# Optimization experiments

Hardware: AMD Instinct MI355X
Metric: run time of the kernel (lower is better)

The kernel has to match this reference:

```python
import jax, jax.numpy as jnp
import numpy as np

HIDDEN = 512
N_LAYERS = 2
SEQ = 512
BATCH = 64
H2 = HIDDEN * 2  # 1024
D_IN = H2 * (N_LAYERS + 1)  # 3072


def setup_inputs() -> dict:
    key = jax.random.key(0)
    ks = jax.random.split(key, 4)
    state = jax.random.normal(ks[0], (N_LAYERS, BATCH, H2), dtype=jnp.float32)
    encoder_output = jax.random.normal(ks[1], (SEQ, BATCH, H2), dtype=jnp.float32)
    # fc1: xavier_normal with tanh gain (5/3); fc2: kaiming_normal
    xavier_std = (5.0 / 3.0) * np.sqrt(2.0 / (D_IN + H2))
    W1 = jax.random.normal(ks[2], (H2, D_IN), dtype=jnp.float32) * xavier_std
    b1 = jnp.zeros((H2,), dtype=jnp.float32)
    W2 = jax.random.normal(ks[3], (1, H2), dtype=jnp.float32) * np.sqrt(2.0 / H2)
    b2 = jnp.zeros((1,), dtype=jnp.float32)
    return {"state": state, "encoder_output": encoder_output,
            "W1": W1, "b1": b1, "W2": W2, "b2": b2}


def reference(state, encoder_output, W1, b1, W2, b2):
    S, B, h2 = encoder_output.shape
    # (n_layers, B, H2) -> (B, n_layers*H2), broadcast over seq
    st = jnp.transpose(state, (1, 0, 2)).reshape(B, -1)
    st = jnp.broadcast_to(st[:, None, :], (B, S, st.shape[-1]))
    enc = jnp.transpose(encoder_output, (1, 0, 2))  # (B, S, H2)
    concat = jnp.concatenate([st, enc], axis=2)      # (B, S, 3*H2)
    energy = jnp.tanh(jnp.einsum('bsd,hd->bsh', concat, W1) + b1)
    energy = (jnp.einsum('bsh,oh->bso', energy, W2) + b2)  # (B, S, 1)
    energy = jnp.transpose(energy, (0, 2, 1))        # (B, 1, S)
    alpha = jax.nn.softmax(energy, axis=2)           # (B, 1, S)
    context = jnp.einsum('bqs,bsh->qbh', alpha, enc)  # (1, B, H2)
    return context, alpha
```

## Files before the change

### kernel.cpp

```cpp
#include <hip/hip_runtime.h>
#include <hip/hip_bf16.h>
#include <stdint.h>

#define H2      1024
#define SEQ     512
#define BATCH   64
#define M_TOTAL (SEQ * BATCH)

typedef __attribute__((ext_vector_type(8))) short short8;
typedef __attribute__((ext_vector_type(4))) float f32x4;

__device__ __forceinline__ unsigned pack2_bf16(float lo, float hi) {
    union { __hip_bfloat162 h; unsigned u; } v;
    v.h = __float22bfloat162_rn(make_float2(lo, hi));
    return v.u;
}

__device__ __forceinline__ float fast_tanh(float x) {
    float e = __expf(2.0f * x);
    return __fdividef(e - 1.0f, e + 1.0f);
}

__device__ __forceinline__ void gl_lds16(const unsigned short* g, unsigned short* l) {
    __builtin_amdgcn_global_load_lds(
        (const __attribute__((address_space(1))) unsigned int*)g,
        (__attribute__((address_space(3))) unsigned int*)l, 16, 0, 0);
}


__global__ __launch_bounds__(256) void k_setup(const float* __restrict__ W1,
                                               const float* __restrict__ b1,
                                               const float* __restrict__ state,
                                               const float* __restrict__ enc,
                                               unsigned short* __restrict__ W1e,
                                               unsigned short* __restrict__ encb,
                                               float* __restrict__ logits,
                                               float* __restrict__ sp,
                                               int swz) {
    int blk = blockIdx.x, tid = threadIdx.x;
    int lane = tid & 63;
    if (blk < 512) {
        if (swz) {
            int gr = blk * 4 + (tid >> 6);
            int L  = ((lane & 3) << 4) | (lane >> 2);
            int h  = ((gr >> 5) << 4) + (L & 15);
            int k  = ((gr & 31) << 5) + ((L >> 4) << 3);
            const float* src = W1 + (size_t)h * 3072 + 2048 + k;
            float4 v0 = *(const float4*)(src);
            float4 v1 = *(const float4*)(src + 4);
            uint4 o;
            o.x = pack2_bf16(v0.x, v0.y); o.y = pack2_bf16(v0.z, v0.w);
            o.z = pack2_bf16(v1.x, v1.y); o.w = pack2_bf16(v1.z, v1.w);
            *(uint4*)(W1e + (size_t)gr * 512 + L * 8) = o;
        } else {
            int i = blk * 256 + tid;
            int e = i << 3;
            int h = e >> 10, k = e & 1023;
            const float* src = W1 + (size_t)h * 3072 + 2048 + k;
            float4 v0 = *(const float4*)(src);
            float4 v1 = *(const float4*)(src + 4);
            uint4 o;
            o.x = pack2_bf16(v0.x, v0.y); o.y = pack2_bf16(v0.z, v0.w);
            o.z = pack2_bf16(v1.x, v1.y); o.w = pack2_bf16(v1.z, v1.w);
            *(uint4*)(W1e + ((size_t)h << 10) + k) = o;
        }
    } else if (blk < 640) {
        logits[(blk - 512) * 256 + tid] = 0.f;
    } else if (blk < 704) {
        int mT   = blk - 640;
        int wave = tid >> 6;
        int c    = lane & 15;
        int kq   = (lane >> 4) << 3;
        int h    = mT * 16 + c;
        int b    = wave * 16 + c;
        const float* ap = W1 + (size_t)h * 3072 + kq;
        f32x4 acc = {0.f, 0.f, 0.f, 0.f};
        #pragma unroll 4
        for (int k0 = 0; k0 < 2048; k0 += 32) {
            int k = k0 + kq;
            float4 a0 = *(const float4*)(ap + k0);
            float4 a1 = *(const float4*)(ap + k0 + 4);
            int l = k >> 10, j = k & 1023;
            const float* bp = state + (((size_t)l * 64 + b) << 10) + j;
            float4 b0 = *(const float4*)bp;
            float4 b1v = *(const float4*)(bp + 4);
            union { short8 s; uint4 u; } fa, fb;
            fa.u.x = pack2_bf16(a0.x, a0.y); fa.u.y = pack2_bf16(a0.z, a0.w);
            fa.u.z = pack2_bf16(a1.x, a1.y); fa.u.w = pack2_bf16(a1.z, a1.w);
            fb.u.x = pack2_bf16(b0.x, b0.y); fb.u.y = pack2_bf16(b0.z, b0.w);
            fb.u.z = pack2_bf16(b1v.x, b1v.y); fb.u.w = pack2_bf16(b1v.z, b1v.w);
            acc = __builtin_amdgcn_mfma_f32_16x16x32_bf16(fa.s, fb.s, acc, 0, 0, 0);
        }
        int quad = lane >> 4;
        int bcol = wave * 16 + c;
        #pragma unroll
        for (int i = 0; i < 4; ++i) {
            int hh = mT * 16 + quad * 4 + i;
            sp[((size_t)bcol << 10) + hh] = acc[i] + b1[hh];
        }
    } else {
        int gr = (blk - 704) * 4 + (tid >> 6);
        int L  = ((lane & 3) << 4) | (lane >> 2);
        int m  = ((gr >> 5) << 4) + (L & 15);
        int k  = ((gr & 31) << 5) + ((L >> 4) << 3);
        const float* src = enc + (size_t)m * 1024 + k;
        float4 v0 = *(const float4*)(src);
        float4 v1 = *(const float4*)(src + 4);
        uint4 o;
        o.x = pack2_bf16(v0.x, v0.y); o.y = pack2_bf16(v0.z, v0.w);
        o.z = pack2_bf16(v1.x, v1.y); o.w = pack2_bf16(v1.z, v1.w);
        *(uint4*)(encb + (size_t)gr * 512 + L * 8) = o;
    }
}

#define BM 128
#define BN 128
#define BK 32

__global__ __launch_bounds__(256, 2) void k_energy(const unsigned short* __restrict__ encb,
                                                   const unsigned short* __restrict__ W1e,
                                                   const float* __restrict__ sp,
                                                   const float* __restrict__ W2,
                                                   float* __restrict__ logits) {
    __shared__ unsigned short As[BM * BK];
    __shared__ unsigned short Bs[BN * BK];
    int bid = blockIdx.x;
    int c8  = bid & 7;
    int jj  = bid >> 3;
    int mT  = c8 * 32 + (jj >> 3);
    int nT  = jj & 7;
    int n0  = nT * BN;
    int m0  = mT * BM;
    int tid  = threadIdx.x;
    int lane = tid & 63, wave = tid >> 6;
    int wm   = (wave >> 1) << 6;
    int wn   = (wave & 1) << 6;

    int rg0 = wave * 2, rg1 = wave * 2 + 1;
    const unsigned short* gA0 = encb + ((size_t)(mT * 8 + rg0) * 32) * 512 + lane * 8;
    const unsigned short* gA1 = encb + ((size_t)(mT * 8 + rg1) * 32) * 512 + lane * 8;
    const unsigned short* gB0 = W1e  + ((size_t)(nT * 8 + rg0) * 32) * 512 + lane * 8;
    const unsigned short* gB1 = W1e  + ((size_t)(nT * 8 + rg1) * 32) * 512 + lane * 8;
    unsigned short* lA0 = As + rg0 * 512;
    unsigned short* lA1 = As + rg1 * 512;
    unsigned short* lB0 = Bs + rg0 * 512;
    unsigned short* lB1 = Bs + rg1 * 512;

    f32x4 acc[4][4];
    #pragma unroll
    for (int mi = 0; mi < 4; ++mi)
        #pragma unroll
        for (int ni = 0; ni < 4; ++ni)
            acc[mi][ni] = (f32x4){0.f, 0.f, 0.f, 0.f};

    int ablk = wm >> 4;
    int bblk = wn >> 4;
    const unsigned short* afb = As + ablk * 512 + lane * 8;
    const unsigned short* bfb = Bs + bblk * 512 + lane * 8;

    for (int k0 = 0; k0 < H2; k0 += BK) {
        int go = k0 * 16;
        __syncthreads();
        gl_lds16(gA0 + go, lA0);
        gl_lds16(gA1 + go, lA1);
        gl_lds16(gB0 + go, lB0);
        gl_lds16(gB1 + go, lB1);
        __syncthreads();
        short8 af[4], bf[4];
        #pragma unroll
        for (int i = 0; i < 4; ++i) {
            af[i] = *(const short8*)(afb + i * 512);
            bf[i] = *(const short8*)(bfb + i * 512);
        }
        #pragma unroll
        for (int mi = 0; mi < 4; ++mi)
            #pragma unroll
            for (int ni = 0; ni < 4; ++ni)
                acc[mi][ni] = __builtin_amdgcn_mfma_f32_16x16x32_bf16(af[mi], bf[ni], acc[mi][ni], 0, 0, 0);
    }

    int c    = lane & 15;
    int quad = lane >> 4;
    float w2v[4];
    int   hcol[4];
    #pragma unroll
    for (int ni = 0; ni < 4; ++ni) {
        hcol[ni] = n0 + wn + ni * 16 + c;
        w2v[ni]  = W2[hcol[ni]];
    }
    #pragma unroll
    for (int mi = 0; mi < 4; ++mi) {
        #pragma unroll
        for (int i = 0; i < 4; ++i) {
            int m = m0 + wm + mi * 16 + quad * 4 + i;
            int b = m & 63;
            const float* sprow = sp + ((size_t)b << 10);
            float t = 0.f;
            #pragma unroll
            for (int ni = 0; ni < 4; ++ni) {
                float e = acc[mi][ni][i] + sprow[hcol[ni]];
                t = fmaf(fast_tanh(e), w2v[ni], t);
            }
            t += __shfl_xor(t, 1);
            t += __shfl_xor(t, 2);
            t += __shfl_xor(t, 4);
            t += __shfl_xor(t, 8);
            if (c == 0) atomicAdd(logits + (size_t)b * 512 + (m >> 6), t);
        }
    }
}

#define LDT 40
__global__ __launch_bounds__(256, 2) void k_energy_f32(const float* __restrict__ enc,
                                                       const unsigned short* __restrict__ W1e,
                                                       const float* __restrict__ sp,
                                                       const float* __restrict__ W2,
                                                       float* __restrict__ logits) {
    __shared__ unsigned short As[BM * LDT];
    __shared__ unsigned short Bs[BN * LDT];
    int bid = blockIdx.x;
    int c8  = bid & 7;
    int jj  = bid >> 3;
    int mT  = c8 * 32 + (jj >> 3);
    int nT  = jj & 7;
    int tid  = threadIdx.x;
    int lane = tid & 63, wave = tid >> 6;
    int wm   = (wave >> 1) << 6;
    int wn   = (wave & 1) << 6;
    int m0   = mT * BM, n0 = nT * BN;

    int arow = tid >> 1;
    int aseg = (tid & 1) << 4;
    const float*          apg = enc + ((size_t)(m0 + arow) << 10) + aseg;
    const unsigned short* wpg = W1e + ((size_t)(n0 + arow) << 10) + aseg;
    unsigned short* asd = As + arow * LDT + aseg;
    unsigned short* bsd = Bs + arow * LDT + aseg;

    f32x4 acc[4][4];
    #pragma unroll
    for (int mi = 0; mi < 4; ++mi)
        #pragma unroll
        for (int ni = 0; ni < 4; ++ni)
            acc[mi][ni] = (f32x4){0.f, 0.f, 0.f, 0.f};

    int c  = lane & 15;
    int kq = (lane >> 4) << 3;
    const unsigned short* afp = As + (wm + c) * LDT + kq;
    const unsigned short* bfp = Bs + (wn + c) * LDT + kq;

    for (int k0 = 0; k0 < 1024; k0 += 32) {
        float4 a0 = *(const float4*)(apg + k0);
        float4 a1 = *(const float4*)(apg + k0 + 4);
        float4 a2 = *(const float4*)(apg + k0 + 8);
        float4 a3 = *(const float4*)(apg + k0 + 12);
        uint4  w0 = *(const uint4*)(wpg + k0);
        uint4  w1 = *(const uint4*)(wpg + k0 + 8);
        uint4 pa0, pa1;
        pa0.x = pack2_bf16(a0.x, a0.y); pa0.y = pack2_bf16(a0.z, a0.w);
        pa0.z = pack2_bf16(a1.x, a1.y); pa0.w = pack2_bf16(a1.z, a1.w);
        pa1.x = pack2_bf16(a2.x, a2.y); pa1.y = pack2_bf16(a2.z, a2.w);
        pa1.z = pack2_bf16(a3.x, a3.y); pa1.w = pack2_bf16(a3.z, a3.w);
        __syncthreads();
        *(uint4*)asd       = pa0;
        *(uint4*)(asd + 8) = pa1;
        *(uint4*)bsd       = w0;
        *(uint4*)(bsd + 8) = w1;
        __syncthreads();
        short8 af[4], bf[4];
        #pragma unroll
        for (int i = 0; i < 4; ++i) {
            af[i] = *(const short8*)(afp + (i << 4) * LDT);
            bf[i] = *(const short8*)(bfp + (i << 4) * LDT);
        }
        #pragma unroll
        for (int mi = 0; mi < 4; ++mi)
            #pragma unroll
            for (int ni = 0; ni < 4; ++ni)
                acc[mi][ni] = __builtin_amdgcn_mfma_f32_16x16x32_bf16(af[mi], bf[ni], acc[mi][ni], 0, 0, 0);
    }

    int quad = lane >> 4;
    float w2v[4];
    int   hcol[4];
    #pragma unroll
    for (int ni = 0; ni < 4; ++ni) {
        hcol[ni] = n0 + wn + ni * 16 + c;
        w2v[ni]  = W2[hcol[ni]];
    }
    #pragma unroll
    for (int mi = 0; mi < 4; ++mi) {
        #pragma unroll
        for (int i = 0; i < 4; ++i) {
            int m = m0 + wm + mi * 16 + quad * 4 + i;
            int b = m & 63;
            const float* sprow = sp + ((size_t)b << 10);
            float t = 0.f;
            #pragma unroll
            for (int ni = 0; ni < 4; ++ni) {
                float e = acc[mi][ni][i] + sprow[hcol[ni]];
                t = fmaf(fast_tanh(e), w2v[ni], t);
            }
            t += __shfl_xor(t, 1);
            t += __shfl_xor(t, 2);
            t += __shfl_xor(t, 4);
            t += __shfl_xor(t, 8);
            if (c == 0) atomicAdd(logits + (size_t)b * 512 + (m >> 6), t);
        }
    }
}

__global__ __launch_bounds__(256) void k_softmax(const float* __restrict__ logits,
                                                 float* __restrict__ alpha,
                                                 float* __restrict__ ctx) {
    int b = blockIdx.x;
    int tid = threadIdx.x;
    int lane = tid & 63, wave = tid >> 6;
    #pragma unroll
    for (int j = 0; j < 4; ++j)
        ctx[((size_t)b << 10) + j * 256 + tid] = 0.f;
    float v0 = logits[(size_t)b * 512 + tid];
    float v1 = logits[(size_t)b * 512 + 256 + tid];
    float mx = fmaxf(v0, v1);
    #pragma unroll
    for (int o = 32; o; o >>= 1) mx = fmaxf(mx, __shfl_xor(mx, o));
    __shared__ float redm[4];
    if (lane == 0) redm[wave] = mx;
    __syncthreads();
    mx = fmaxf(fmaxf(redm[0], redm[1]), fmaxf(redm[2], redm[3]));
    float e0 = __expf(v0 - mx), e1 = __expf(v1 - mx);
    float s = e0 + e1;
    #pragma unroll
    for (int o = 32; o; o >>= 1) s += __shfl_xor(s, o);
    __shared__ float reds[4];
    if (lane == 0) reds[wave] = s;
    __syncthreads();
    s = reds[0] + reds[1] + reds[2] + reds[3];
    float inv = 1.0f / s;
    alpha[(size_t)b * 512 + tid]       = e0 * inv;
    alpha[(size_t)b * 512 + 256 + tid] = e1 * inv;
}

__global__ __launch_bounds__(256) void k_context(const float* __restrict__ enc,
                                                 const float* __restrict__ alpha,
                                                 float* __restrict__ ctx) {
    int b  = blockIdx.x & 63;
    int sc = blockIdx.x >> 6;
    int h  = threadIdx.x << 2;
    float4 acc = make_float4(0.f, 0.f, 0.f, 0.f);
    int sbase = sc * 64;
    #pragma unroll 4
    for (int si = 0; si < 64; ++si) {
        int s = sbase + si;
        float a = alpha[(size_t)b * 512 + s];
        float4 e = *(const float4*)(enc + (((size_t)s * 64 + b) << 10) + h);
        acc.x = fmaf(a, e.x, acc.x);
        acc.y = fmaf(a, e.y, acc.y);
        acc.z = fmaf(a, e.z, acc.z);
        acc.w = fmaf(a, e.w, acc.w);
    }
    float* dst = ctx + ((size_t)b << 10) + h;
    atomicAdd(dst + 0, acc.x);
    atomicAdd(dst + 1, acc.y);
    atomicAdd(dst + 2, acc.z);
    atomicAdd(dst + 3, acc.w);
}

extern "C" void kernel_launch(void* const* d_in, const int* in_sizes, int n_in,
                              void* d_out, int out_size, void* d_ws, size_t ws_size,
                              hipStream_t stream) {
    const float* state = (const float*)d_in[0];
    const float* enc   = (const float*)d_in[1];
    const float* W1    = (const float*)d_in[2];
    const float* b1    = (const float*)d_in[3];
    const float* W2    = (const float*)d_in[4];

    float* ctx   = (float*)d_out;
    float* alpha = (float*)d_out + 65536;

    char* ws = (char*)d_ws;
    unsigned short* W1e    = (unsigned short*)(ws);
    float*          sp     = (float*)(ws + 2097152);
    float*          logits = (float*)(ws + 2097152 + 262144);
    unsigned short* encb   = (unsigned short*)(ws + 2097152 + 262144 + 131072);

    const size_t need_full = 2097152 + 262144 + 131072 + (size_t)M_TOTAL * H2 * 2;
    bool full = ws_size >= need_full;

    k_setup<<<full ? 17088 : 704, 256, 0, stream>>>(W1, b1, state, enc, W1e, encb,
                                                    logits, sp, full ? 1 : 0);
    if (full) {
        k_energy<<<M_TOTAL / BM * (H2 / BN), 256, 0, stream>>>(encb, W1e, sp, W2, logits);
    } else {
        k_energy_f32<<<M_TOTAL / BM * (H2 / BN), 256, 0, stream>>>(enc, W1e, sp, W2, logits);
    }
    k_softmax<<<64, 256, 0, stream>>>(logits, alpha, ctx);
    k_context<<<512, 256, 0, stream>>>(enc, alpha, ctx);
}
```

Baseline: 384.3 us.

## Fuse fp32-to-bf16 conversion of encoder output into energy GEMM A-tile loads

Removes the separate pass in the setup kernel that converted the full encoder output (64 MB fp32) into a swizzled bf16 buffer. The energy GEMM now reads fp32 encoder rows directly, converts them to bf16 in registers and writes them to LDS, with next-iteration A loads issued as register prefetch to overlap the MFMA work. This drops a 64 MB read plus 32 MB write round trip, but each energy block now reads fp32 A (twice the bytes, repeated across the 8 N-tiles) and adds conversion ALU work inside the main loop. The fallback fp32 energy kernel and the workspace-size switch are removed.

New measurement: 436.4 us. 13.5% more time.

```diff
diff --git a/kernel.cpp b/kernel.cpp
--- a/kernel.cpp
+++ b/kernel.cpp
@@ -31,42 +31,26 @@
 __global__ __launch_bounds__(256) void k_setup(const float* __restrict__ W1,
                                                const float* __restrict__ b1,
                                                const float* __restrict__ state,
-                                               const float* __restrict__ enc,
                                                unsigned short* __restrict__ W1e,
-                                               unsigned short* __restrict__ encb,
                                                float* __restrict__ logits,
-                                               float* __restrict__ sp,
-                                               int swz) {
+                                               float* __restrict__ sp) {
     int blk = blockIdx.x, tid = threadIdx.x;
     int lane = tid & 63;
     if (blk < 512) {
-        if (swz) {
-            int gr = blk * 4 + (tid >> 6);
-            int L  = ((lane & 3) << 4) | (lane >> 2);
-            int h  = ((gr >> 5) << 4) + (L & 15);
-            int k  = ((gr & 31) << 5) + ((L >> 4) << 3);
-            const float* src = W1 + (size_t)h * 3072 + 2048 + k;
-            float4 v0 = *(const float4*)(src);
-            float4 v1 = *(const float4*)(src + 4);
-            uint4 o;
-            o.x = pack2_bf16(v0.x, v0.y); o.y = pack2_bf16(v0.z, v0.w);
-            o.z = pack2_bf16(v1.x, v1.y); o.w = pack2_bf16(v1.z, v1.w);
-            *(uint4*)(W1e + (size_t)gr * 512 + L * 8) = o;
-        } else {
-            int i = blk * 256 + tid;
-            int e = i << 3;
-            int h = e >> 10, k = e & 1023;
-            const float* src = W1 + (size_t)h * 3072 + 2048 + k;
-            float4 v0 = *(const float4*)(src);
-            float4 v1 = *(const float4*)(src + 4);
-            uint4 o;
-            o.x = pack2_bf16(v0.x, v0.y); o.y = pack2_bf16(v0.z, v0.w);
-            o.z = pack2_bf16(v1.x, v1.y); o.w = pack2_bf16(v1.z, v1.w);
-            *(uint4*)(W1e + ((size_t)h << 10) + k) = o;
-        }
+        int gr = blk * 4 + (tid >> 6);
+        int L  = ((lane & 3) << 4) | (lane >> 2);
+        int h  = ((gr >> 5) << 4) + (L & 15);
+        int k  = ((gr & 31) << 5) + ((L >> 4) << 3);
+        const float* src = W1 + (size_t)h * 3072 + 2048 + k;
+        float4 v0 = *(const float4*)(src);
+        float4 v1 = *(const float4*)(src + 4);
+        uint4 o;
+        o.x = pack2_bf16(v0.x, v0.y); o.y = pack2_bf16(v0.z, v0.w);
+        o.z = pack2_bf16(v1.x, v1.y); o.w = pack2_bf16(v1.z, v1.w);
+        *(uint4*)(W1e + (size_t)gr * 512 + L * 8) = o;
     } else if (blk < 640) {
         logits[(blk - 512) * 256 + tid] = 0.f;
-    } else if (blk < 704) {
+    } else {
         int mT   = blk - 640;
         int wave = tid >> 6;
         int c    = lane & 15;
@@ -98,18 +82,6 @@
             int hh = mT * 16 + quad * 4 + i;
             sp[((size_t)bcol << 10) + hh] = acc[i] + b1[hh];
         }
-    } else {
-        int gr = (blk - 704) * 4 + (tid >> 6);
-        int L  = ((lane & 3) << 4) | (lane >> 2);
-        int m  = ((gr >> 5) << 4) + (L & 15);
-        int k  = ((gr & 31) << 5) + ((L >> 4) << 3);
-        const float* src = enc + (size_t)m * 1024 + k;
-        float4 v0 = *(const float4*)(src);
-        float4 v1 = *(const float4*)(src + 4);
-        uint4 o;
-        o.x = pack2_bf16(v0.x, v0.y); o.y = pack2_bf16(v0.z, v0.w);
-        o.z = pack2_bf16(v1.x, v1.y); o.w = pack2_bf16(v1.z, v1.w);
-        *(uint4*)(encb + (size_t)gr * 512 + L * 8) = o;
     }
 }
 
@@ -117,7 +89,7 @@
 #define BN 128
 #define BK 32
 
-__global__ __launch_bounds__(256, 2) void k_energy(const unsigned short* __restrict__ encb,
+__global__ __launch_bounds__(256, 2) void k_energy(const float* __restrict__ enc,
                                                    const unsigned short* __restrict__ W1e,
                                                    const float* __restrict__ sp,
                                                    const float* __restrict__ W2,
@@ -137,12 +109,15 @@
     int wn   = (wave & 1) << 6;
 
     int rg0 = wave * 2, rg1 = wave * 2 + 1;
-    const unsigned short* gA0 = encb + ((size_t)(mT * 8 + rg0) * 32) * 512 + lane * 8;
-    const unsigned short* gA1 = encb + ((size_t)(mT * 8 + rg1) * 32) * 512 + lane * 8;
-    const unsigned short* gB0 = W1e  + ((size_t)(nT * 8 + rg0) * 32) * 512 + lane * 8;
-    const unsigned short* gB1 = W1e  + ((size_t)(nT * 8 + rg1) * 32) * 512 + lane * 8;
-    unsigned short* lA0 = As + rg0 * 512;
-    unsigned short* lA1 = As + rg1 * 512;
+    int arow0 = m0 + rg0 * 16 + (lane & 15);
+    int arow1 = m0 + rg1 * 16 + (lane & 15);
+    int akoff = (lane >> 4) << 3;
+    const float* gA0 = enc + (size_t)arow0 * 1024 + akoff;
+    const float* gA1 = enc + (size_t)arow1 * 1024 + akoff;
+    const unsigned short* gB0 = W1e + ((size_t)(nT * 8 + rg0) * 32) * 512 + lane * 8;
+    const unsigned short* gB1 = W1e + ((size_t)(nT * 8 + rg1) * 32) * 512 + lane * 8;
+    unsigned short* lA0 = As + rg0 * 512 + lane * 8;
+    unsigned short* lA1 = As + rg1 * 512 + lane * 8;
     unsigned short* lB0 = Bs + rg0 * 512;
     unsigned short* lB1 = Bs + rg1 * 512;
 
@@ -158,14 +133,29 @@
     const unsigned short* afb = As + ablk * 512 + lane * 8;
     const unsigned short* bfb = Bs + bblk * 512 + lane * 8;
 
+    float4 a00 = *(const float4*)(gA0);
+    float4 a01 = *(const float4*)(gA0 + 4);
+    float4 a10 = *(const float4*)(gA1);
+    float4 a11 = *(const float4*)(gA1 + 4);
+
     for (int k0 = 0; k0 < H2; k0 += BK) {
         int go = k0 * 16;
         __syncthreads();
-        gl_lds16(gA0 + go, lA0);
-        gl_lds16(gA1 + go, lA1);
+        uint4 w0, w1;
+        w0.x = pack2_bf16(a00.x, a00.y); w0.y = pack2_bf16(a00.z, a00.w);
+        w0.z = pack2_bf16(a01.x, a01.y); w0.w = pack2_bf16(a01.z, a01.w);
+        w1.x = pack2_bf16(a10.x, a10.y); w1.y = pack2_bf16(a10.z, a10.w);
+        w1.z = pack2_bf16(a11.x, a11.y); w1.w = pack2_bf16(a11.z, a11.w);
+        *(uint4*)lA0 = w0;
+        *(uint4*)lA1 = w1;
         gl_lds16(gB0 + go, lB0);
         gl_lds16(gB1 + go, lB1);
         __syncthreads();
+        int kn = (k0 + BK) & (H2 - 1);
+        float4 t00 = *(const float4*)(gA0 + kn);
+        float4 t01 = *(const float4*)(gA0 + kn + 4);
+        float4 t10 = *(const float4*)(gA1 + kn);
+        float4 t11 = *(const float4*)(gA1 + kn + 4);
         short8 af[4], bf[4];
         #pragma unroll
         for (int i = 0; i < 4; ++i) {
@@ -177,108 +167,10 @@
             #pragma unroll
             for (int ni = 0; ni < 4; ++ni)
                 acc[mi][ni] = __builtin_amdgcn_mfma_f32_16x16x32_bf16(af[mi], bf[ni], acc[mi][ni], 0, 0, 0);
+        a00 = t00; a01 = t01; a10 = t10; a11 = t11;
     }
 
     int c    = lane & 15;
-    int quad = lane >> 4;
-    float w2v[4];
-    int   hcol[4];
-    #pragma unroll
-    for (int ni = 0; ni < 4; ++ni) {
-        hcol[ni] = n0 + wn + ni * 16 + c;
-        w2v[ni]  = W2[hcol[ni]];
-    }
-    #pragma unroll
-    for (int mi = 0; mi < 4; ++mi) {
-        #pragma unroll
-        for (int i = 0; i < 4; ++i) {
-            int m = m0 + wm + mi * 16 + quad * 4 + i;
-            int b = m & 63;
-            const float* sprow = sp + ((size_t)b << 10);
-            float t = 0.f;
-            #pragma unroll
-            for (int ni = 0; ni < 4; ++ni) {
-                float e = acc[mi][ni][i] + sprow[hcol[ni]];
-                t = fmaf(fast_tanh(e), w2v[ni], t);
-            }
-            t += __shfl_xor(t, 1);
-            t += __shfl_xor(t, 2);
-            t += __shfl_xor(t, 4);
-            t += __shfl_xor(t, 8);
-            if (c == 0) atomicAdd(logits + (size_t)b * 512 + (m >> 6), t);
-        }
-    }
-}
-
-#define LDT 40
-__global__ __launch_bounds__(256, 2) void k_energy_f32(const float* __restrict__ enc,
-                                                       const unsigned short* __restrict__ W1e,
-                                                       const float* __restrict__ sp,
-                                                       const float* __restrict__ W2,
-                                                       float* __restrict__ logits) {
-    __shared__ unsigned short As[BM * LDT];
-    __shared__ unsigned short Bs[BN * LDT];
-    int bid = blockIdx.x;
-    int c8  = bid & 7;
-    int jj  = bid >> 3;
-    int mT  = c8 * 32 + (jj >> 3);
-    int nT  = jj & 7;
-    int tid  = threadIdx.x;
-    int lane = tid & 63, wave = tid >> 6;
-    int wm   = (wave >> 1) << 6;
-    int wn   = (wave & 1) << 6;
-    int m0   = mT * BM, n0 = nT * BN;
-
-    int arow = tid >> 1;
-    int aseg = (tid & 1) << 4;
-    const float*          apg = enc + ((size_t)(m0 + arow) << 10) + aseg;
-    const unsigned short* wpg = W1e + ((size_t)(n0 + arow) << 10) + aseg;
-    unsigned short* asd = As + arow * LDT + aseg;
-    unsigned short* bsd = Bs + arow * LDT + aseg;
-
-    f32x4 acc[4][4];
-    #pragma unroll
-    for (int mi = 0; mi < 4; ++mi)
-        #pragma unroll
-        for (int ni = 0; ni < 4; ++ni)
-            acc[mi][ni] = (f32x4){0.f, 0.f, 0.f, 0.f};
-
-    int c  = lane & 15;
-    int kq = (lane >> 4) << 3;
-    const unsigned short* afp = As + (wm + c) * LDT + kq;
-    const unsigned short* bfp = Bs + (wn + c) * LDT + kq;
-
-    for (int k0 = 0; k0 < 1024; k0 += 32) {
-        float4 a0 = *(const float4*)(apg + k0);
-        float4 a1 = *(const float4*)(apg + k0 + 4);
-        float4 a2 = *(const float4*)(apg + k0 + 8);
-        float4 a3 = *(const float4*)(apg + k0 + 12);
-        uint4  w0 = *(const uint4*)(wpg + k0);
-        uint4  w1 = *(const uint4*)(wpg + k0 + 8);
-        uint4 pa0, pa1;
-        pa0.x = pack2_bf16(a0.x, a0.y); pa0.y = pack2_bf16(a0.z, a0.w);
-        pa0.z = pack2_bf16(a1.x, a1.y); pa0.w = pack2_bf16(a1.z, a1.w);
-        pa1.x = pack2_bf16(a2.x, a2.y); pa1.y = pack2_bf16(a2.z, a2.w);
-        pa1.z = pack2_bf16(a3.x, a3.y); pa1.w = pack2_bf16(a3.z, a3.w);
-        __syncthreads();
-        *(uint4*)asd       = pa0;
-        *(uint4*)(asd + 8) = pa1;
-        *(uint4*)bsd       = w0;
-        *(uint4*)(bsd + 8) = w1;
-        __syncthreads();
-        short8 af[4], bf[4];
-        #pragma unroll
-        for (int i = 0; i < 4; ++i) {
-            af[i] = *(const short8*)(afp + (i << 4) * LDT);
-            bf[i] = *(const short8*)(bfp + (i << 4) * LDT);
-        }
-        #pragma unroll
-        for (int mi = 0; mi < 4; ++mi)
-            #pragma unroll
-            for (int ni = 0; ni < 4; ++ni)
-                acc[mi][ni] = __builtin_amdgcn_mfma_f32_16x16x32_bf16(af[mi], bf[ni], acc[mi][ni], 0, 0, 0);
-    }
-
     int quad = lane >> 4;
     float w2v[4];
     int   hcol[4];
@@ -381,18 +273,9 @@
     unsigned short* W1e    = (unsigned short*)(ws);
     float*          sp     = (float*)(ws + 2097152);
     float*          logits = (float*)(ws + 2097152 + 262144);
-    unsigned short* encb   = (unsigned short*)(ws + 2097152 + 262144 + 131072);
-
-    const size_t need_full = 2097152 + 262144 + 131072 + (size_t)M_TOTAL * H2 * 2;
-    bool full = ws_size >= need_full;
-
-    k_setup<<<full ? 17088 : 704, 256, 0, stream>>>(W1, b1, state, enc, W1e, encb,
-                                                    logits, sp, full ? 1 : 0);
-    if (full) {
-        k_energy<<<M_TOTAL / BM * (H2 / BN), 256, 0, stream>>>(encb, W1e, sp, W2, logits);
-    } else {
-        k_energy_f32<<<M_TOTAL / BM * (H2 / BN), 256, 0, stream>>>(enc, W1e, sp, W2, logits);
-    }
+
+    k_setup<<<704, 256, 0, stream>>>(W1, b1, state, W1e, logits, sp);
+    k_energy<<<M_TOTAL / BM * (H2 / BN), 256, 0, stream>>>(enc, W1e, sp, W2, logits);
     k_softmax<<<64, 256, 0, stream>>>(logits, alpha, ctx);
     k_context<<<512, 256, 0, stream>>>(enc, alpha, ctx);
 }
```
